# Kernel tuning notes

Hardware: AMD Instinct MI355X
Metric: run time of the kernel (lower is better)

Reference implementation:

```python
import jax, jax.numpy as jnp
import numpy as np

DIM = 1024
NUM_HEADS = 32
HEAD_DIM = 32
T = 2048
SCALE = 0.12
ROT_BASE = HEAD_DIM * 4  # Rotary(head_dim, max_seq_len, head_dim*4)
RMS_EPS = 1.1920929e-07  # torch float32 finfo eps (F.rms_norm default)


def _rms_norm(x):
    ms = jnp.mean(jnp.square(x), axis=-1, keepdims=True)
    return x * jax.lax.rsqrt(ms + RMS_EPS)


def _rotary_tables(seq_len):
    # modded-nanogpt half-truncated rotary: frequencies on first quarter, zeros on second
    quarter = HEAD_DIM // 4
    af = (1.0 / ROT_BASE) ** jnp.linspace(0.0, 1.0, quarter, dtype=jnp.float32)
    af = jnp.concatenate([af, jnp.zeros(quarter, dtype=jnp.float32)])  # [hd/2]
    theta = jnp.arange(seq_len, dtype=jnp.float32)[:, None] * af[None, :]  # [T, hd/2]
    return jnp.cos(theta), jnp.sin(theta)


def _apply_rotary(x, cos, sin):
    # x: [B, T, H, hd]; cos/sin: [T, hd/2]
    x1, x2 = jnp.split(x, 2, axis=-1)
    c = cos[None, :, None, :]
    s = sin[None, :, None, :]
    y1 = x1 * c + x2 * s
    y2 = -x1 * s + x2 * c
    return jnp.concatenate([y1, y2], axis=-1)


def setup_inputs() -> dict:
    key = jax.random.key(0)
    k1, k2, k3, k4 = jax.random.split(key, 4)
    std = 0.5 * DIM ** (-0.5)
    bound = (3.0 ** 0.5) * std
    x = jax.random.normal(k1, (1, T, DIM), dtype=jnp.float32)
    ve = jax.random.normal(k2, (1, T, NUM_HEADS * HEAD_DIM), dtype=jnp.float32)
    qkv_w = jax.random.uniform(k3, (3, NUM_HEADS * HEAD_DIM, DIM), dtype=jnp.float32,
                               minval=-bound, maxval=bound)
    lambdas = jnp.array([0.5, 0.5], dtype=jnp.float32)
    # original zero-inits c_proj; use small random so output/grads are nontrivial
    c_proj_w = jax.random.normal(k4, (DIM, NUM_HEADS * HEAD_DIM), dtype=jnp.float32) * 0.02
    return {"x": x, "ve": ve, "qkv_w": qkv_w, "lambdas": lambdas, "c_proj_w": c_proj_w}


def reference(x, ve, qkv_w, lambdas, c_proj_w):
    B, T_, D = x.shape
    H, hd = NUM_HEADS, HEAD_DIM
    # fused QKV projection: F.linear(x, qkv_w.flatten(end_dim=1))
    w = qkv_w.reshape(3 * H * hd, D)
    qkv = jnp.einsum('btd,ed->bte', x, w).reshape(B, T_, 3 * H, hd)
    q, k, v = jnp.split(qkv, 3, axis=2)  # each [B, T, H, hd]
    q = _rms_norm(q)
    k = _rms_norm(k)
    cos, sin = _rotary_tables(T_)
    q = _apply_rotary(q, cos, sin)
    k = _apply_rotary(k, cos, sin)
    v = lambdas[0] * v + lambdas[1] * ve.reshape(B, T_, H, hd)
    # causal attention with fixed scale 0.12
    scores = jnp.einsum('bqhd,bkhd->bhqk', q, k) * SCALE
    causal = jnp.tril(jnp.ones((T_, T_), dtype=bool))
    scores = jnp.where(causal[None, None, :, :], scores, -jnp.inf)
    attn = jax.nn.softmax(scores, axis=-1)
    y = jnp.einsum('bhqk,bkhd->bqhd', attn, v).reshape(B, T_, H * hd)
    return jnp.einsum('bte,de->btd', y, c_proj_w)
```

## Files before the change

### kernel.cpp

```cpp
#include <hip/hip_runtime.h>
#include <hip/hip_bf16.h>

#define NHEADS 32
#define HD_ 32
#define TSEQ 2048
#define SCALE_ 0.12f
#define LOG2E_ 1.44269504088896f
#define RMS_EPS_ 1.1920929e-07f

typedef unsigned short ushort_t;
typedef __bf16 bf16_t;
typedef __attribute__((ext_vector_type(8))) bf16_t bf16x8;
typedef __attribute__((ext_vector_type(4))) float f32x4;
typedef __attribute__((ext_vector_type(8))) unsigned short u16x8;

__device__ __forceinline__ ushort_t f2bfn(float f){
    __hip_bfloat16 b = __float2bfloat16(f);
    return *reinterpret_cast<ushort_t*>(&b);
}
__device__ __forceinline__ float bf2f(ushort_t s){
    union { unsigned u; float f; } v; v.u = ((unsigned)s) << 16;
    return v.f;
}
__device__ __forceinline__ float fexp2(float x){
#if __has_builtin(__builtin_amdgcn_exp2f)
    return __builtin_amdgcn_exp2f(x);
#else
    return exp2f(x);
#endif
}
__device__ __forceinline__ void gld16(const void* g, void* l){
    __builtin_amdgcn_global_load_lds(
        (const __attribute__((address_space(1))) unsigned int*)g,
        (__attribute__((address_space(3))) unsigned int*)l,
        16, 0, 0);
}

__global__ __launch_bounds__(256) void k_prep(const float* __restrict__ x,
                                              const float* __restrict__ qkw,
                                              const float* __restrict__ cpw,
                                              ushort_t* __restrict__ xb,
                                              ushort_t* __restrict__ wb,
                                              ushort_t* __restrict__ cpb,
                                              float* __restrict__ cost,
                                              float* __restrict__ sint)
{
    const int n1 = TSEQ * 1024 / 4, n2 = 3 * 1024 * 1024 / 4, n3 = 1024 * 1024 / 4;
    int i = blockIdx.x * 256 + threadIdx.x;
    if (i < n1 + n2 + n3){
        const float* src; ushort_t* dst; int j = i;
        if (j < n1){ src = x; dst = xb; }
        else if (j < n1 + n2){ j -= n1; src = qkw; dst = wb; }
        else { j -= n1 + n2; src = cpw; dst = cpb; }
        float4 v = ((const float4*)src)[j];
        ushort4 o;
        o.x = f2bfn(v.x); o.y = f2bfn(v.y); o.z = f2bfn(v.z); o.w = f2bfn(v.w);
        ((ushort4*)dst)[j] = o;
    } else {
        int g = i - (n1 + n2 + n3);
        if (g < TSEQ * 16){
            int t = g >> 4, ii = g & 15;
            float c = 1.0f, s = 0.0f;
            if (ii < 8){
                float af = powf(1.0f / 128.0f, (float)ii * (1.0f / 7.0f));
                sincosf((float)t * af, &s, &c);
            }
            cost[g] = c; sint[g] = s;
        }
    }
}

__global__ __launch_bounds__(256, 3) void k_gemm_qkv(const ushort_t* __restrict__ A,
                                                     const ushort_t* __restrict__ B,
                                                     const float* __restrict__ ve,
                                                     const float* __restrict__ lam,
                                                     const float* __restrict__ cost,
                                                     const float* __restrict__ sint,
                                                     ushort_t* __restrict__ qb,
                                                     ushort_t* __restrict__ kbuf,
                                                     ushort_t* __restrict__ vtb)
{
    const int K = 1024;
    __shared__ __align__(16) ushort_t As[2][128 * 32];
    __shared__ __align__(16) ushort_t Bs[2][64 * 32];
    const int tid = threadIdx.x;
    const int lane = tid & 63;
    const int w = tid >> 6;
    const int wr = w >> 1, wc = w & 1;
    const int l15 = lane & 15, hi = lane >> 4;
    const int m0 = blockIdx.y * 128, n0 = blockIdx.x * 64;
    const int sec = n0 >> 10;
    const int h = ((n0 & 1023) >> 5) + wc;
    const int srow = lane >> 2, scol = (lane & 3) * 8;

    f32x4 acc[4][2] = {};

    auto stage = [&](int k0, int buf){
        #pragma unroll
        for (int i = 0; i < 2; ++i){
            int c = w + i * 4;
            gld16(&A[(size_t)(m0 + c * 16 + srow) * K + k0 + scol], &As[buf][c * 512]);
        }
        gld16(&B[(size_t)(n0 + w * 16 + srow) * K + k0 + scol], &Bs[buf][w * 512]);
    };

    stage(0, 0);
    int cur = 0;
    for (int k0 = 0; k0 < K; k0 += 32){
        __syncthreads();
        if (k0 + 32 < K) stage(k0 + 32, cur ^ 1);
        bf16x8 af[4], bfr[2];
        #pragma unroll
        for (int mi = 0; mi < 4; ++mi)
            af[mi] = *(const bf16x8*)&As[cur][(wr * 64 + mi * 16 + l15) * 32 + hi * 8];
        #pragma unroll
        for (int ni = 0; ni < 2; ++ni)
            bfr[ni] = *(const bf16x8*)&Bs[cur][(wc * 32 + ni * 16 + l15) * 32 + hi * 8];
        #pragma unroll
        for (int mi = 0; mi < 4; ++mi)
            #pragma unroll
            for (int ni = 0; ni < 2; ++ni)
                acc[mi][ni] = __builtin_amdgcn_mfma_f32_16x16x32_bf16(af[mi], bfr[ni], acc[mi][ni], 0, 0, 0);
        cur ^= 1;
    }

    if (sec < 2){
        ushort_t* dst = (sec == 0) ? qb : kbuf;
        const float qscl = (sec == 0) ? SCALE_ * LOG2E_ : 1.0f;
        #pragma unroll
        for (int mi = 0; mi < 4; ++mi){
            #pragma unroll
            for (int r = 0; r < 4; ++r){
                const int t = m0 + wr * 64 + mi * 16 + hi * 4 + r;
                float v0 = acc[mi][0][r], v1 = acc[mi][1][r];
                float ss = v0 * v0 + v1 * v1;
                ss += __shfl_xor(ss, 1);
                ss += __shfl_xor(ss, 2);
                ss += __shfl_xor(ss, 4);
                ss += __shfl_xor(ss, 8);
                const float inv = rsqrtf(ss * (1.0f / 32.0f) + RMS_EPS_);
                const float c = cost[t * 16 + l15], s = sint[t * 16 + l15];
                const float n0v = v0 * inv, n1v = v1 * inv;
                const float o0 = (n0v * c + n1v * s) * qscl;
                const float o1 = (n1v * c - n0v * s) * qscl;
                size_t base = ((size_t)h * TSEQ + t) * 32;
                dst[base + l15]      = f2bfn(o0);
                dst[base + 16 + l15] = f2bfn(o1);
            }
        }
    } else {
        const float l0 = lam[0], l1 = lam[1];
        __syncthreads();
        ushort_t* vt = &As[0][0] + w * 2048;
        #pragma unroll
        for (int ni = 0; ni < 2; ++ni){
            const int d = ni * 16 + l15;
            #pragma unroll
            for (int mi = 0; mi < 4; ++mi){
                #pragma unroll
                for (int r = 0; r < 4; ++r){
                    const int t = m0 + wr * 64 + mi * 16 + hi * 4 + r;
                    const int tl = mi * 16 + hi * 4 + r;
                    float vef = ve[(size_t)t * 1024 + h * 32 + d];
                    float ov = l0 * acc[mi][ni][r] + l1 * vef;
                    const int g = (tl >> 3) ^ (d & 7);
                    vt[d * 64 + g * 8 + (tl & 7)] = f2bfn(ov);
                }
            }
        }
        __syncthreads();
        const int tc = lane & 7;
        #pragma unroll
        for (int p = 0; p < 4; ++p){
            const int d = p * 8 + (lane >> 3);
            const int g = tc ^ (d & 7);
            u16x8 o = *(const u16x8*)&vt[d * 64 + g * 8];
            *(u16x8*)&vtb[((size_t)h * HD_ + d) * TSEQ + m0 + wr * 64 + tc * 8] = o;
        }
    }
}

__global__ __launch_bounds__(256) void k_gemm_out(const ushort_t* __restrict__ A,
                                                  const ushort_t* __restrict__ B,
                                                  float* __restrict__ C,
                                                  int M, int N, int K)
{
    __shared__ __align__(16) ushort_t As[2][64 * 64];
    __shared__ __align__(16) ushort_t Bs[2][64 * 64];
    const int tid = threadIdx.x;
    const int lane = tid & 63;
    const int w = tid >> 6;
    const int wr = w >> 1, wc = w & 1;
    const int l15 = lane & 15, hi = lane >> 4;
    const int m0 = blockIdx.y * 64, n0 = blockIdx.x * 64;
    const int srow = lane >> 3, scol = (lane & 7) * 8;

    f32x4 acc[2][2] = {};

    auto stage = [&](int k0, int buf){
        #pragma unroll
        for (int i = 0; i < 2; ++i){
            int c = w * 2 + i;
            gld16(&A[(size_t)(m0 + c * 8 + srow) * K + k0 + scol], &As[buf][c * 512]);
            gld16(&B[(size_t)(n0 + c * 8 + srow) * K + k0 + scol], &Bs[buf][c * 512]);
        }
    };

    stage(0, 0);
    int cur = 0;
    for (int k0 = 0; k0 < K; k0 += 64){
        __syncthreads();
        if (k0 + 64 < K) stage(k0 + 64, cur ^ 1);
        bf16x8 af[2][2], bfr[2][2];
        #pragma unroll
        for (int mi = 0; mi < 2; ++mi)
            #pragma unroll
            for (int sub = 0; sub < 2; ++sub)
                af[mi][sub] = *(const bf16x8*)&As[cur][(wr * 32 + mi * 16 + l15) * 64 + sub * 32 + hi * 8];
        #pragma unroll
        for (int ni = 0; ni < 2; ++ni)
            #pragma unroll
            for (int sub = 0; sub < 2; ++sub)
                bfr[ni][sub] = *(const bf16x8*)&Bs[cur][(wc * 32 + ni * 16 + l15) * 64 + sub * 32 + hi * 8];
        #pragma unroll
        for (int sub = 0; sub < 2; ++sub)
            #pragma unroll
            for (int mi = 0; mi < 2; ++mi)
                #pragma unroll
                for (int ni = 0; ni < 2; ++ni)
                    acc[mi][ni] = __builtin_amdgcn_mfma_f32_16x16x32_bf16(af[mi][sub], bfr[ni][sub], acc[mi][ni], 0, 0, 0);
        cur ^= 1;
    }

    #pragma unroll
    for (int mi = 0; mi < 2; ++mi)
        #pragma unroll
        for (int ni = 0; ni < 2; ++ni)
            #pragma unroll
            for (int r = 0; r < 4; ++r){
                int row = m0 + wr * 32 + mi * 16 + hi * 4 + r;
                int col = n0 + wc * 32 + ni * 16 + l15;
                C[(size_t)row * N + col] = acc[mi][ni][r];
            }
}

template<bool MASK>
__device__ __forceinline__ void chain_step(const bf16x8* kf, const bf16x8* vv0, const bf16x8* vv1,
                                           ushort_t* pb, const bf16x8& qf,
                                           int kb0, int qrow, int l15, int hi,
                                           f32x4& a0, f32x4& a1, float& lp)
{
    f32x4 s[4];
    __builtin_amdgcn_s_setprio(1);
    #pragma unroll
    for (int ni = 0; ni < 4; ++ni){
        f32x4 z = {0.f, 0.f, 0.f, 0.f};
        s[ni] = __builtin_amdgcn_mfma_f32_16x16x32_bf16(kf[ni], qf, z, 0, 0, 0);
    }
    __builtin_amdgcn_s_setprio(0);
    if (MASK){
        const int relc = qrow - kb0 - 4 * hi;
        #pragma unroll
        for (int ni = 0; ni < 4; ++ni)
            #pragma unroll
            for (int r = 0; r < 4; ++r)
                if (16 * ni + r > relc) s[ni][r] = -1e30f;
    }
    float ps = 0.f;
    #pragma unroll
    for (int ni = 0; ni < 4; ++ni)
        #pragma unroll
        for (int r = 0; r < 4; ++r){
            float p = fexp2(s[ni][r]);
            s[ni][r] = p;
            ps += p;
        }
    lp += ps;
    #pragma unroll
    for (int ni = 0; ni < 4; ++ni){
        ushort4 pk;
        pk.x = f2bfn(s[ni][0]); pk.y = f2bfn(s[ni][1]);
        pk.z = f2bfn(s[ni][2]); pk.w = f2bfn(s[ni][3]);
        *(ushort4*)&pb[l15 * 72 + ni * 16 + hi * 4] = pk;
    }
    __builtin_amdgcn_s_setprio(1);
    #pragma unroll
    for (int kk = 0; kk < 2; ++kk){
        bf16x8 pf = *(const bf16x8*)&pb[l15 * 72 + kk * 32 + hi * 8];
        a0 = __builtin_amdgcn_mfma_f32_16x16x32_bf16(vv0[kk], pf, a0, 0, 0, 0);
        a1 = __builtin_amdgcn_mfma_f32_16x16x32_bf16(vv1[kk], pf, a1, 0, 0, 0);
    }
    __builtin_amdgcn_s_setprio(0);
}

__global__ __launch_bounds__(256) void k_attn(const ushort_t* __restrict__ qb,
                                              const ushort_t* __restrict__ kb,
                                              const ushort_t* __restrict__ vtb,
                                              ushort_t* __restrict__ yb)
{
    const int bid = blockIdx.x;
    const int xcd = bid & 7, idx = bid >> 3;
    const int h = xcd * 4 + (idx >> 4);
    const int b = idx & 15;
    const int tid = threadIdx.x;
    const int w = tid >> 6, lane = tid & 63;
    const int l15 = lane & 15, hi = lane >> 4;

    __shared__ __align__(16) ushort_t Kbuf[2][128 * 32];
    __shared__ __align__(16) ushort_t Vbuf[2][32 * 128];
    __shared__ __align__(16) ushort_t Pbuf[4][16 * 72];

    const ushort_t* kb_h = kb + (size_t)h * TSEQ * HD_;
    const ushort_t* vt_h = vtb + (size_t)h * HD_ * TSEQ;
    const ushort_t* qb_h = qb + (size_t)h * TSEQ * HD_;

    const int qtA = b, qtB = 31 - b;
    const int qwA = qtA * 64 + w * 16, qwB = qtB * 64 + w * 16;
    const bf16x8 qfA = *(const bf16x8*)&qb_h[(size_t)(qwA + l15) * 32 + hi * 8];
    const bf16x8 qfB = *(const bf16x8*)&qb_h[(size_t)(qwB + l15) * 32 + hi * 8];

    const int kck0 = w * 2;
    auto stage = [&](int bs, int buf){
        const int kb0 = bs * 128;
        #pragma unroll
        for (int i = 0; i < 2; ++i){
            int c = kck0 + i;
            int krow = c * 16 + (lane >> 2);
            gld16(&kb_h[(size_t)(kb0 + krow) * 32 + (lane & 3) * 8], &Kbuf[buf][c * 512]);
            int vrow = c * 4 + (lane >> 4);
            int vj = (lane & 15) ^ (vrow & 7);
            gld16(&vt_h[(size_t)vrow * TSEQ + kb0 + vj * 8], &Vbuf[buf][c * 512]);
        }
    };

    f32x4 a0A = {0.f,0.f,0.f,0.f}, a1A = a0A, a0B = a0A, a1B = a0A;
    float lpA = 0.f, lpB = 0.f;
    ushort_t* pb = &Pbuf[w][0];

    const int nB = qtB + 1;
    const int NB2 = (nB + 1) >> 1;

    stage(0, 0);
    int cur = 0;
    for (int bs = 0; bs < NB2; ++bs){
        __syncthreads();
        if (bs + 1 < NB2) stage(bs + 1, cur ^ 1);
        #pragma unroll
        for (int sub = 0; sub < 2; ++sub){
            const int kt = bs * 2 + sub;
            if (kt >= nB) break;
            const int kb0 = kt * 64;
            bf16x8 kf[4], vv0[2], vv1[2];
            #pragma unroll
            for (int ni = 0; ni < 4; ++ni)
                kf[ni] = *(const bf16x8*)&Kbuf[cur][(sub * 64 + ni * 16 + l15) * 32 + hi * 8];
            #pragma unroll
            for (int kk = 0; kk < 2; ++kk){
                int sl = sub * 8 + kk * 4 + hi;
                vv0[kk] = *(const bf16x8*)&Vbuf[cur][l15 * 128 + (sl ^ (l15 & 7)) * 8];
                vv1[kk] = *(const bf16x8*)&Vbuf[cur][(16 + l15) * 128 + (sl ^ (l15 & 7)) * 8];
            }
            if (kt < qtB)
                chain_step<false>(kf, vv0, vv1, pb, qfB, kb0, qwB + l15, l15, hi, a0B, a1B, lpB);
            else
                chain_step<true >(kf, vv0, vv1, pb, qfB, kb0, qwB + l15, l15, hi, a0B, a1B, lpB);
            if (kt < qtA)
                chain_step<false>(kf, vv0, vv1, pb, qfA, kb0, qwA + l15, l15, hi, a0A, a1A, lpA);
            else if (kt == qtA)
                chain_step<true >(kf, vv0, vv1, pb, qfA, kb0, qwA + l15, l15, hi, a0A, a1A, lpA);
        }
        cur ^= 1;
    }

    #pragma unroll
    for (int which = 0; which < 2; ++which){
        f32x4 a0 = which ? a0B : a0A;
        f32x4 a1 = which ? a1B : a1A;
        float lp = which ? lpB : lpA;
        int qw = which ? qwB : qwA;
        lp += __shfl_xor(lp, 16);
        lp += __shfl_xor(lp, 32);
        float inv = 1.0f / lp;
        ushort4 o0, o1;
        o0.x = f2bfn(a0[0]*inv); o0.y = f2bfn(a0[1]*inv);
        o0.z = f2bfn(a0[2]*inv); o0.w = f2bfn(a0[3]*inv);
        o1.x = f2bfn(a1[0]*inv); o1.y = f2bfn(a1[1]*inv);
        o1.z = f2bfn(a1[2]*inv); o1.w = f2bfn(a1[3]*inv);
        size_t base = (size_t)(qw + l15) * 1024 + h * 32;
        *(ushort4*)&yb[base + hi * 4]      = o0;
        *(ushort4*)&yb[base + 16 + hi * 4] = o1;
    }
}

extern "C" void kernel_launch(void* const* d_in, const int* in_sizes, int n_in,
                              void* d_out, int out_size, void* d_ws, size_t ws_size,
                              hipStream_t stream)
{
    const float* x   = (const float*)d_in[0];
    const float* ve  = (const float*)d_in[1];
    const float* qkw = (const float*)d_in[2];
    const float* lam = (const float*)d_in[3];
    const float* cpw = (const float*)d_in[4];

    char* ws = (char*)d_ws;
    size_t o = 0;
    auto take = [&](size_t bytes) -> char* {
        char* p = ws + o; o += (bytes + 255) & ~(size_t)255; return p;
    };
    ushort_t* xb   = (ushort_t*)take((size_t)TSEQ * 1024 * 2);
    ushort_t* wb   = (ushort_t*)take((size_t)3072 * 1024 * 2);
    ushort_t* cpb  = (ushort_t*)take((size_t)1024 * 1024 * 2);
    float*    cost = (float*)take((size_t)TSEQ * 16 * 4);
    float*    sint = (float*)take((size_t)TSEQ * 16 * 4);
    ushort_t* qb   = (ushort_t*)take((size_t)NHEADS * TSEQ * HD_ * 2);
    ushort_t* kb   = (ushort_t*)take((size_t)NHEADS * TSEQ * HD_ * 2 + 8192);
    ushort_t* vtb  = (ushort_t*)take((size_t)NHEADS * HD_ * TSEQ * 2 + 8192);
    ushort_t* yb   = xb;

    const int prep_items = (TSEQ * 1024 + 3 * 1024 * 1024 + 1024 * 1024) / 4 + TSEQ * 16;
    k_prep<<<(prep_items + 255) / 256, 256, 0, stream>>>(x, qkw, cpw, xb, wb, cpb, cost, sint);
    k_gemm_qkv<<<dim3(48, 16), 256, 0, stream>>>(xb, wb, ve, lam, cost, sint, qb, kb, vtb);
    k_attn<<<512, 256, 0, stream>>>(qb, kb, vtb, yb);
    k_gemm_out<<<dim3(1024 / 64, TSEQ / 64), 256, 0, stream>>>(yb, cpb, (float*)d_out, TSEQ, 1024, 1024);
}
```

Measured before the change: 153.2 us.

## Split paired-tile attention blocks into one q-tile per block, heaviest first

The attention kernel previously paired q-tiles b and 31-b in one block, sharing each K/V stage across both. Now each block handles a single 64-row q-tile, with 1024 blocks ordered longest-first. K/V staging tiles shrink to 64 keys and launch bounds request 4 blocks per CU. This aims for more parallelism and better occupancy. In exchange, K/V loads per tile are no longer shared across two q-tiles, and load balance now depends on the scheduler rather than on the fixed pairing.

```diff
diff --git a/kernel.cpp b/kernel.cpp
--- a/kernel.cpp
+++ b/kernel.cpp
@@ -293,103 +293,79 @@
     __builtin_amdgcn_s_setprio(0);
 }
 
-__global__ __launch_bounds__(256) void k_attn(const ushort_t* __restrict__ qb,
-                                              const ushort_t* __restrict__ kb,
-                                              const ushort_t* __restrict__ vtb,
-                                              ushort_t* __restrict__ yb)
+__global__ __launch_bounds__(256, 4) void k_attn(const ushort_t* __restrict__ qb,
+                                                 const ushort_t* __restrict__ kb,
+                                                 const ushort_t* __restrict__ vtb,
+                                                 ushort_t* __restrict__ yb)
 {
     const int bid = blockIdx.x;
     const int xcd = bid & 7, idx = bid >> 3;
-    const int h = xcd * 4 + (idx >> 4);
-    const int b = idx & 15;
+    const int h  = xcd * 4 + (idx & 3);
+    const int qt = 31 - (idx >> 2);
     const int tid = threadIdx.x;
     const int w = tid >> 6, lane = tid & 63;
     const int l15 = lane & 15, hi = lane >> 4;
 
-    __shared__ __align__(16) ushort_t Kbuf[2][128 * 32];
-    __shared__ __align__(16) ushort_t Vbuf[2][32 * 128];
+    __shared__ __align__(16) ushort_t Kbuf[2][64 * 32];
+    __shared__ __align__(16) ushort_t Vbuf[2][32 * 64];
     __shared__ __align__(16) ushort_t Pbuf[4][16 * 72];
 
     const ushort_t* kb_h = kb + (size_t)h * TSEQ * HD_;
     const ushort_t* vt_h = vtb + (size_t)h * HD_ * TSEQ;
     const ushort_t* qb_h = qb + (size_t)h * TSEQ * HD_;
 
-    const int qtA = b, qtB = 31 - b;
-    const int qwA = qtA * 64 + w * 16, qwB = qtB * 64 + w * 16;
-    const bf16x8 qfA = *(const bf16x8*)&qb_h[(size_t)(qwA + l15) * 32 + hi * 8];
-    const bf16x8 qfB = *(const bf16x8*)&qb_h[(size_t)(qwB + l15) * 32 + hi * 8];
-
-    const int kck0 = w * 2;
-    auto stage = [&](int bs, int buf){
-        const int kb0 = bs * 128;
-        #pragma unroll
-        for (int i = 0; i < 2; ++i){
-            int c = kck0 + i;
-            int krow = c * 16 + (lane >> 2);
-            gld16(&kb_h[(size_t)(kb0 + krow) * 32 + (lane & 3) * 8], &Kbuf[buf][c * 512]);
-            int vrow = c * 4 + (lane >> 4);
-            int vj = (lane & 15) ^ (vrow & 7);
-            gld16(&vt_h[(size_t)vrow * TSEQ + kb0 + vj * 8], &Vbuf[buf][c * 512]);
-        }
+    const int qw = qt * 64 + w * 16;
+    const bf16x8 qf = *(const bf16x8*)&qb_h[(size_t)(qw + l15) * 32 + hi * 8];
+
+    const int krow = w * 16 + (lane >> 2);
+    const int kcol = (lane & 3) * 8;
+    const int vrow = w * 8 + (lane >> 3);
+    const int vslot = (lane & 7) ^ (vrow & 7);
+    auto stage = [&](int kt, int buf){
+        const int kb0 = kt * 64;
+        gld16(&kb_h[(size_t)(kb0 + krow) * 32 + kcol], &Kbuf[buf][w * 512]);
+        gld16(&vt_h[(size_t)vrow * TSEQ + kb0 + vslot * 8], &Vbuf[buf][w * 512]);
     };
 
-    f32x4 a0A = {0.f,0.f,0.f,0.f}, a1A = a0A, a0B = a0A, a1B = a0A;
-    float lpA = 0.f, lpB = 0.f;
+    f32x4 a0 = {0.f,0.f,0.f,0.f}, a1 = a0;
+    float lp = 0.f;
     ushort_t* pb = &Pbuf[w][0];
 
-    const int nB = qtB + 1;
-    const int NB2 = (nB + 1) >> 1;
-
+    const int nT = qt + 1;
     stage(0, 0);
     int cur = 0;
-    for (int bs = 0; bs < NB2; ++bs){
+    for (int kt = 0; kt < nT; ++kt){
         __syncthreads();
-        if (bs + 1 < NB2) stage(bs + 1, cur ^ 1);
-        #pragma unroll
-        for (int sub = 0; sub < 2; ++sub){
-            const int kt = bs * 2 + sub;
-            if (kt >= nB) break;
-            const int kb0 = kt * 64;
-            bf16x8 kf[4], vv0[2], vv1[2];
-            #pragma unroll
-            for (int ni = 0; ni < 4; ++ni)
-                kf[ni] = *(const bf16x8*)&Kbuf[cur][(sub * 64 + ni * 16 + l15) * 32 + hi * 8];
-            #pragma unroll
-            for (int kk = 0; kk < 2; ++kk){
-                int sl = sub * 8 + kk * 4 + hi;
-                vv0[kk] = *(const bf16x8*)&Vbuf[cur][l15 * 128 + (sl ^ (l15 & 7)) * 8];
-                vv1[kk] = *(const bf16x8*)&Vbuf[cur][(16 + l15) * 128 + (sl ^ (l15 & 7)) * 8];
-            }
-            if (kt < qtB)
-                chain_step<false>(kf, vv0, vv1, pb, qfB, kb0, qwB + l15, l15, hi, a0B, a1B, lpB);
-            else
-                chain_step<true >(kf, vv0, vv1, pb, qfB, kb0, qwB + l15, l15, hi, a0B, a1B, lpB);
-            if (kt < qtA)
-                chain_step<false>(kf, vv0, vv1, pb, qfA, kb0, qwA + l15, l15, hi, a0A, a1A, lpA);
-            else if (kt == qtA)
-                chain_step<true >(kf, vv0, vv1, pb, qfA, kb0, qwA + l15, l15, hi, a0A, a1A, lpA);
-        }
+        if (kt + 1 < nT) stage(kt + 1, cur ^ 1);
+        const int kb0 = kt * 64;
+        bf16x8 kf[4], vv0[2], vv1[2];
+        #pragma unroll
+        for (int ni = 0; ni < 4; ++ni)
+            kf[ni] = *(const bf16x8*)&Kbuf[cur][(ni * 16 + l15) * 32 + hi * 8];
+        #pragma unroll
+        for (int kk = 0; kk < 2; ++kk){
+            int sl = kk * 4 + hi;
+            vv0[kk] = *(const bf16x8*)&Vbuf[cur][l15 * 64 + (sl ^ (l15 & 7)) * 8];
+            vv1[kk] = *(const bf16x8*)&Vbuf[cur][(16 + l15) * 64 + (sl ^ (l15 & 7)) * 8];
+        }
+        if (kt < qt)
+            chain_step<false>(kf, vv0, vv1, pb, qf, kb0, qw + l15, l15, hi, a0, a1, lp);
+        else
+            chain_step<true >(kf, vv0, vv1, pb, qf, kb0, qw + l15, l15, hi, a0, a1, lp);
         cur ^= 1;
     }
 
-    #pragma unroll
-    for (int which = 0; which < 2; ++which){
-        f32x4 a0 = which ? a0B : a0A;
-        f32x4 a1 = which ? a1B : a1A;
-        float lp = which ? lpB : lpA;
-        int qw = which ? qwB : qwA;
-        lp += __shfl_xor(lp, 16);
-        lp += __shfl_xor(lp, 32);
-        float inv = 1.0f / lp;
-        ushort4 o0, o1;
-        o0.x = f2bfn(a0[0]*inv); o0.y = f2bfn(a0[1]*inv);
-        o0.z = f2bfn(a0[2]*inv); o0.w = f2bfn(a0[3]*inv);
-        o1.x = f2bfn(a1[0]*inv); o1.y = f2bfn(a1[1]*inv);
-        o1.z = f2bfn(a1[2]*inv); o1.w = f2bfn(a1[3]*inv);
-        size_t base = (size_t)(qw + l15) * 1024 + h * 32;
-        *(ushort4*)&yb[base + hi * 4]      = o0;
-        *(ushort4*)&yb[base + 16 + hi * 4] = o1;
-    }
+    lp += __shfl_xor(lp, 16);
+    lp += __shfl_xor(lp, 32);
+    float inv = 1.0f / lp;
+    ushort4 o0, o1;
+    o0.x = f2bfn(a0[0]*inv); o0.y = f2bfn(a0[1]*inv);
+    o0.z = f2bfn(a0[2]*inv); o0.w = f2bfn(a0[3]*inv);
+    o1.x = f2bfn(a1[0]*inv); o1.y = f2bfn(a1[1]*inv);
+    o1.z = f2bfn(a1[2]*inv); o1.w = f2bfn(a1[3]*inv);
+    size_t base = (size_t)(qw + l15) * 1024 + h * 32;
+    *(ushort4*)&yb[base + hi * 4]      = o0;
+    *(ushort4*)&yb[base + 16 + hi * 4] = o1;
 }
 
 extern "C" void kernel_launch(void* const* d_in, const int* in_sizes, int n_in,
@@ -420,6 +396,6 @@
     const int prep_items = (TSEQ * 1024 + 3 * 1024 * 1024 + 1024 * 1024) / 4 + TSEQ * 16;
     k_prep<<<(prep_items + 255) / 256, 256, 0, stream>>>(x, qkw, cpw, xb, wb, cpb, cost, sint);
     k_gemm_qkv<<<dim3(48, 16), 256, 0, stream>>>(xb, wb, ve, lam, cost, sint, qb, kb, vtb);
-    k_attn<<<512, 256, 0, stream>>>(qb, kb, vtb, yb);
+    k_attn<<<1024, 256, 0, stream>>>(qb, kb, vtb, yb);
     k_gemm_out<<<dim3(1024 / 64, TSEQ / 64), 256, 0, stream>>>(yb, cpb, (float*)d_out, TSEQ, 1024, 1024);
 }
```

After: 152.0 us. Within noise of the previous version (-0.8%).
